# Kernel optimization log

Hardware: AMD Instinct MI355X
Metric: run time of the kernel (lower is better)

Reference implementation:

```python
import jax, jax.numpy as jnp
import numpy as np


def setup_inputs() -> dict:
    key = jax.random.key(0)
    k1, k2 = jax.random.split(key)
    B, N, D = 16, 2048, 256      # batch, tokens, token_dim
    C, K = 8, 1024               # num_codebooks, num_tokens
    x_in = jax.random.normal(k1, (B, N, D), dtype=jnp.float32)
    # torch.rand init for each VQCodebook embedding -> uniform[0,1)
    codebooks = jax.random.uniform(k2, (C, K, D), dtype=jnp.float32)
    return {"x_in": x_in, "codebooks": codebooks}


def _apply_one_codebook(x_res, emb, code_sg):
    d2 = (
        jnp.sum(x_res * x_res, axis=-1, keepdims=True)
        - 2.0 * jnp.einsum("bnd,kd->bnk", x_res, emb)
        + jnp.sum(emb * emb, axis=-1)
    )
    idx = jnp.argmin(d2, axis=-1)          # (B,N)
    z_q = emb[idx]                         # (B,N,D) gather
    if code_sg:                            # straight-through estimator
        z_q = x_res + jax.lax.stop_gradient(z_q - x_res)
    return z_q, idx


def reference(x_in, codebooks, code_sg=True):
    C = codebooks.shape[0]
    x_res = x_in
    z_q = jnp.zeros_like(x_in)
    idx_list = []
    for i in range(C):  # sequential residual dependency, loop over fixed num_codebooks
        # faithful to original: subtracts CUMULATIVE z_q each iteration
        x_res = x_res - z_q
        z_q_i, idx_i = _apply_one_codebook(x_res, codebooks[i], code_sg)
        z_q = z_q + z_q_i
        idx_list.append(idx_i)
    indices = jnp.stack(idx_list, axis=-2)  # (B, C, N)
    return z_q, indices
```

## Files before the change

kernel.cpp:

```cpp
#include <hip/hip_runtime.h>
#include <cstdint>

#define TOKENS   32768
#define DIM      256
#define KCB      1024
#define CBOOKS   8
#define NTOK     2048
#define ZQ_ELEMS (TOKENS * DIM)
#define EPS_GAP  2.0e-2f

typedef _Float16 f16x8 __attribute__((ext_vector_type(8)));
typedef float    f32x4 __attribute__((ext_vector_type(4)));

__device__ float np_pairwise_sumsq_256(const float4* a4) {
  #pragma clang fp contract(off)
  float h[2];
  for (int hh = 0; hh < 2; ++hh) {
    const float4* b = a4 + hh * 32;
    float4 v0 = b[0], v1 = b[1];
    float r0 = v0.x * v0.x, r1 = v0.y * v0.y, r2 = v0.z * v0.z, r3 = v0.w * v0.w;
    float r4 = v1.x * v1.x, r5 = v1.y * v1.y, r6 = v1.z * v1.z, r7 = v1.w * v1.w;
    for (int t = 1; t < 16; ++t) {
      float4 w0 = b[2 * t], w1 = b[2 * t + 1];
      r0 = r0 + w0.x * w0.x; r1 = r1 + w0.y * w0.y;
      r2 = r2 + w0.z * w0.z; r3 = r3 + w0.w * w0.w;
      r4 = r4 + w1.x * w1.x; r5 = r5 + w1.y * w1.y;
      r6 = r6 + w1.z * w1.z; r7 = r7 + w1.w * w1.w;
    }
    h[hh] = ((r0 + r1) + (r2 + r3)) + ((r4 + r5) + (r6 + r7));
  }
  return h[0] + h[1];
}

__device__ __forceinline__ float4 f4_muladd(float4 a, float4 b, float4 c) {
  #pragma clang fp contract(off)
  float4 r;
  r.x = a.x * b.x + c.x;
  r.y = a.y * b.y + c.y;
  r.z = a.z * b.z + c.z;
  r.w = a.w * b.w + c.w;
  return r;
}

__global__ __launch_bounds__(256) void rvq_norms_kernel(
    const float* __restrict__ cb, float* __restrict__ sume) {
  int row = blockIdx.x * 256 + threadIdx.x;
  sume[row] = np_pairwise_sumsq_256((const float4*)&cb[(size_t)row * DIM]);
}

__global__ __launch_bounds__(256) void rvq_efsplit_kernel(
    const float* __restrict__ cbc, f16x8* __restrict__ EfC,
    int* __restrict__ fix_cnt) {
  if (blockIdx.x == 0 && threadIdx.x == 0) *fix_cnt = 0;
  int gw = blockIdx.x * 4 + (threadIdx.x >> 6);
  int l  = threadIdx.x & 63;
  int row = gw * 16 + (l & 15);
  #pragma unroll
  for (int kb = 0; kb < 8; ++kb) {
    int d0 = kb * 32 + ((l >> 4) << 3);
    float4 u = *(const float4*)&cbc[(size_t)row * DIM + d0];
    float4 v = *(const float4*)&cbc[(size_t)row * DIM + d0 + 4];
    float ev[8] = {u.x, u.y, u.z, u.w, v.x, v.y, v.z, v.w};
    f16x8 hi, lo;
    #pragma unroll
    for (int i = 0; i < 8; ++i) {
      _Float16 h = (_Float16)ev[i];
      hi[i] = h; lo[i] = (_Float16)(ev[i] - (float)h);
    }
    EfC[((size_t)gw * 16 + kb) * 64 + l]     = hi;
    EfC[((size_t)gw * 16 + kb + 8) * 64 + l] = lo;
  }
}

__global__ __launch_bounds__(256, 2) void rvq_screen_kernel(
    const float* __restrict__ xr, const f16x8* __restrict__ EfC,
    const float* __restrict__ sume, int* __restrict__ idx_ws,
    int* __restrict__ fix_list, int* __restrict__ fix_cnt,
    float* __restrict__ idxf) {
  __shared__ f16x8 ldsB[2][2][8][2][64];

  const int tid  = threadIdx.x;
  const int lane = tid & 63;
  const int w    = tid >> 6;
  const int m0w  = blockIdx.x * 64 + w * 16;

  f16x8 ah[8], al[8];
  {
    const float* base = &xr[(size_t)(m0w + (lane & 15)) * DIM + ((lane >> 4) << 3)];
    #pragma unroll
    for (int kc = 0; kc < 8; ++kc) {
      float4 u = *(const float4*)(base + kc * 32);
      float4 v = *(const float4*)(base + kc * 32 + 4);
      float xv[8] = {u.x, u.y, u.z, u.w, v.x, v.y, v.z, v.w};
      #pragma unroll
      for (int i = 0; i < 8; ++i) {
        _Float16 h = (_Float16)xv[i];
        ah[kc][i] = h; al[kc][i] = (_Float16)(xv[i] - (float)h);
      }
    }
  }

  float rv1[4], rv2[4]; int ri1[4];
  #pragma unroll
  for (int r = 0; r < 4; ++r) { rv1[r] = 3.0e38f; rv2[r] = 3.0e38f; ri1[r] = 0x7fffffff; }

#define STAGE_B(BUF, NT, KCB_)                                               \
  { _Pragma("unroll")                                                        \
    for (int cc = 0; cc < 8; ++cc) {                                         \
      int p = cc * 4 + w;                                                    \
      int half = p & 1, ni = (p >> 1) & 7, kcw = p >> 4;                     \
      const f16x8* src =                                                     \
          &EfC[(((size_t)(NT) * 8 + ni) * 16 + (KCB_) + kcw + (half ? 8 : 0))\
               * 64 + lane];                                                 \
      __builtin_amdgcn_global_load_lds(                                      \
          (const __attribute__((address_space(1))) uint32_t*)src,            \
          (__attribute__((address_space(3))) uint32_t*)&ldsB[BUF][kcw][ni][half][0], \
          16, 0, 0);                                                         \
    } }

#define MFMA_CHUNK(BUF, KCB_)                                                \
  { _Pragma("unroll")                                                        \
    for (int kcw = 0; kcw < 2; ++kcw) {                                      \
      _Pragma("unroll")                                                      \
      for (int ni = 0; ni < 8; ++ni) {                                       \
        f16x8 bh = ldsB[BUF][kcw][ni][0][lane];                              \
        f16x8 bl = ldsB[BUF][kcw][ni][1][lane];                              \
        acc[ni] = __builtin_amdgcn_mfma_f32_16x16x32_f16(                    \
            ah[(KCB_) + kcw], bh, acc[ni], 0, 0, 0);                         \
        acc[ni] = __builtin_amdgcn_mfma_f32_16x16x32_f16(                    \
            al[(KCB_) + kcw], bh, acc[ni], 0, 0, 0);                         \
        acc[ni] = __builtin_amdgcn_mfma_f32_16x16x32_f16(                    \
            ah[(KCB_) + kcw], bl, acc[ni], 0, 0, 0);                         \
      }                                                                      \
    } }

  f32x4 acc[8];
  #pragma unroll
  for (int ni = 0; ni < 8; ++ni) acc[ni] = (f32x4){0.f, 0.f, 0.f, 0.f};

  STAGE_B(0, 0, 0)
  __syncthreads();

  #pragma unroll 1
  for (int ntile = 0; ntile < 8; ++ntile) {
    #pragma unroll
    for (int chunk = 0; chunk < 4; ++chunk) {
      const int buf = chunk & 1;
      if (ntile * 4 + chunk < 31) {
        int nt2  = (chunk < 3) ? ntile : ntile + 1;
        int kcb2 = ((chunk + 1) & 3) * 2;
        STAGE_B(buf ^ 1, nt2, kcb2)
      }
      MFMA_CHUNK(buf, chunk * 2)
      __syncthreads();
    }
    const int n0 = ntile * 128;
    float se[8];
    #pragma unroll
    for (int ni = 0; ni < 8; ++ni) se[ni] = sume[n0 + ni * 16 + (lane & 15)];
    #pragma unroll
    for (int r = 0; r < 4; ++r) {
      float v1 = 3.0e38f, v2 = 3.0e38f; int i1 = 0x7fffffff;
      #pragma unroll
      for (int ni = 0; ni < 8; ++ni) {
        float key = fmaf(-2.0f, acc[ni][r], se[ni]);
        int   k   = n0 + ni * 16 + (lane & 15);
        if (key < v1 || (key == v1 && k < i1)) { v2 = v1; v1 = key; i1 = k; }
        else { v2 = fminf(v2, key); }
      }
      #pragma unroll
      for (int off = 1; off < 16; off <<= 1) {
        float ov1 = __shfl_xor(v1, off, 64);
        int   oi1 = __shfl_xor(i1, off, 64);
        float ov2 = __shfl_xor(v2, off, 64);
        if (ov1 < v1 || (ov1 == v1 && oi1 < i1)) { v2 = fminf(ov2, v1); v1 = ov1; i1 = oi1; }
        else { v2 = fminf(v2, fminf(ov1, ov2)); }
      }
      if (v1 < rv1[r] || (v1 == rv1[r] && i1 < ri1[r])) {
        rv2[r] = fminf(rv1[r], v2); rv1[r] = v1; ri1[r] = i1;
      } else { rv2[r] = fminf(rv2[r], fminf(v1, v2)); }
    }
    #pragma unroll
    for (int ni = 0; ni < 8; ++ni) acc[ni] = (f32x4){0.f, 0.f, 0.f, 0.f};
  }
#undef STAGE_B
#undef MFMA_CHUNK

  if ((lane & 15) == 0) {
    #pragma unroll
    for (int r = 0; r < 4; ++r) {
      int token = m0w + (lane >> 4) * 4 + r;
      idx_ws[token] = ri1[r];
      if (rv2[r] - rv1[r] < EPS_GAP) {
        int pos = atomicAdd(fix_cnt, 1);
        fix_list[pos] = token;
      }
      int b = token >> 11, n = token & (NTOK - 1);
      idxf[(size_t)b * (CBOOKS * NTOK) + n] = (float)ri1[r];
    }
  }
}

__global__ __launch_bounds__(256, 2) void rvq_fixup_kernel(
    const float* __restrict__ xr, const float* __restrict__ cbc,
    const float* __restrict__ sume, const int* __restrict__ fix_list,
    const int* __restrict__ fix_cnt, int* __restrict__ idx_ws,
    float* __restrict__ idxf) {
  #pragma clang fp contract(off)
  __shared__ float xs[DIM];
  __shared__ float redv[4];
  __shared__ int   redi[4];
  __shared__ float sxv_sh;
  const int tid  = threadIdx.x;
  const int nfix = *fix_cnt;

  #pragma unroll 1
  for (int i = blockIdx.x; i < nfix; i += gridDim.x) {
    int token = fix_list[i];
    __syncthreads();
    if (tid < 64)
      ((float4*)xs)[tid] = ((const float4*)xr)[(size_t)token * 64 + tid];
    __syncthreads();
    if (tid < 64) {
      float s = 0.f;
      if ((tid & 63) < 16) {
        int j = tid & 7, hh = (tid >> 3) & 1;
        const float* bb = xs + hh * 128;
        float r = bb[j] * bb[j];
        #pragma unroll 1
        for (int t = 1; t < 16; ++t) r = r + bb[8 * t + j] * bb[8 * t + j];
        s = r;
      }
      #pragma unroll
      for (int off = 1; off <= 8; off <<= 1)
        s = s + __shfl_xor(s, off, 64);
      if (tid == 0) sxv_sh = s;
    }
    __syncthreads();
    float sxv = sxv_sh;
    float bv = 3.0e38f; int bi = 0x7fffffff;
    #pragma unroll 1
    for (int kk = 0; kk < 4; ++kk) {
      int k = kk * 256 + tid;
      float4 vacc = {0.f, 0.f, 0.f, 0.f};
      #pragma unroll 1
      for (int t = 0; t < 16; ++t) {
        float4 ab = vacc;
        #pragma unroll
        for (int j = 3; j >= 0; --j) {
          float4 xq = *(const float4*)&xs[t * 16 + j * 4];
          float4 eq = *(const float4*)&cbc[(size_t)k * DIM + t * 16 + j * 4];
          ab = f4_muladd(xq, eq, ab);
        }
        vacc = ab;
      }
      float dot = (vacc.x + vacc.y) + (vacc.z + vacc.w);
      float d2  = (sxv - 2.0f * dot) + sume[k];
      if (d2 < bv || (d2 == bv && k < bi)) { bv = d2; bi = k; }
    }
    #pragma unroll
    for (int off = 1; off < 64; off <<= 1) {
      float ov = __shfl_xor(bv, off, 64);
      int   oi = __shfl_xor(bi, off, 64);
      if (ov < bv || (ov == bv && oi < bi)) { bv = ov; bi = oi; }
    }
    int w = tid >> 6;
    if ((tid & 63) == 0) { redv[w] = bv; redi[w] = bi; }
    __syncthreads();
    if (tid == 0) {
      #pragma unroll
      for (int ww = 1; ww < 4; ++ww)
        if (redv[ww] < bv || (redv[ww] == bv && redi[ww] < bi)) { bv = redv[ww]; bi = redi[ww]; }
      idx_ws[token] = bi;
      int b = token >> 11, n = token & (NTOK - 1);
      idxf[(size_t)b * (CBOOKS * NTOK) + n] = (float)bi;
    }
  }
}

__global__ __launch_bounds__(256) void rvq_zq_resid_kernel(
    const float* __restrict__ xsrc, const float* __restrict__ cbc,
    const int* __restrict__ idx_ws, float* __restrict__ zq,
    float* __restrict__ xdst, int first, int last) {
  #pragma clang fp contract(off)
  int gid   = blockIdx.x * 256 + threadIdx.x;
  int token = gid >> 6;
  int q     = gid & 63;
  int idx   = idx_ws[token];
  float4 e = ((const float4*)cbc)[(size_t)idx * 64 + q];
  float4 x = ((const float4*)xsrc)[gid];
  float4 zi;
  zi.x = x.x + (e.x - x.x); zi.y = x.y + (e.y - x.y);
  zi.z = x.z + (e.z - x.z); zi.w = x.w + (e.w - x.w);
  float4 zo;
  if (first) { zo = zi; }
  else {
    float4 z = ((float4*)zq)[gid];
    zo.x = z.x + zi.x; zo.y = z.y + zi.y; zo.z = z.z + zi.z; zo.w = z.w + zi.w;
  }
  ((float4*)zq)[gid] = zo;
  if (!last) {
    float4 xn;
    xn.x = x.x - zo.x; xn.y = x.y - zo.y; xn.z = x.z - zo.z; xn.w = x.w - zo.w;
    ((float4*)xdst)[gid] = xn;
  }
}

extern "C" void kernel_launch(void* const* d_in, const int* in_sizes, int n_in,
                              void* d_out, int out_size, void* d_ws, size_t ws_size,
                              hipStream_t stream) {
  const float* x_in = (const float*)d_in[0];
  const float* cbs  = (const float*)d_in[1];
  float* zq      = (float*)d_out;
  float* idxbase = (float*)d_out + ZQ_ELEMS;

  char* ws = (char*)d_ws;
  float*  sume     = (float*)ws;
  int*    idx_ws   = (int*)(ws + (256 << 10));
  int*    fix_list = (int*)(ws + (448 << 10));
  int*    fix_cnt  = (int*)(ws + (640 << 10));
  f16x8*  EfC      = (f16x8*)(ws + (5 << 20));
  float*  xr       = (float*)(ws + (8 << 20));

  rvq_norms_kernel<<<32, 256, 0, stream>>>(cbs, sume);
  for (int c = 0; c < CBOOKS; ++c) {
    const float* src = (c == 0) ? x_in : xr;
    const float* cbc = cbs + (size_t)c * KCB * DIM;
    float* idxf = idxbase + (size_t)c * NTOK;
    rvq_efsplit_kernel<<<16, 256, 0, stream>>>(cbc, EfC, fix_cnt);
    rvq_screen_kernel<<<512, 256, 0, stream>>>(
        src, EfC, sume + (size_t)c * KCB, idx_ws, fix_list, fix_cnt, idxf);
    rvq_fixup_kernel<<<256, 256, 0, stream>>>(
        src, cbc, sume + (size_t)c * KCB, fix_list, fix_cnt, idx_ws, idxf);
    rvq_zq_resid_kernel<<<8192, 256, 0, stream>>>(
        src, cbc, idx_ws, zq, xr, c == 0, c == CBOOKS - 1);
  }
}
```

Measured before the change: 1.005 ms.

## Fuse z_q accumulation and residual update into the next screen kernel's prologue

```diff
diff --git a/kernel.cpp b/kernel.cpp
--- a/kernel.cpp
+++ b/kernel.cpp
@@ -73,10 +73,11 @@
 }
 
 __global__ __launch_bounds__(256, 2) void rvq_screen_kernel(
-    const float* __restrict__ xr, const f16x8* __restrict__ EfC,
-    const float* __restrict__ sume, int* __restrict__ idx_ws,
-    int* __restrict__ fix_list, int* __restrict__ fix_cnt,
-    float* __restrict__ idxf) {
+    const float* __restrict__ xsrc, const float* __restrict__ cbp,
+    const f16x8* __restrict__ EfC, const float* __restrict__ sume,
+    int* __restrict__ idx_ws, int* __restrict__ fix_list,
+    int* __restrict__ fix_cnt, float* __restrict__ idxf,
+    float* __restrict__ zq, float* __restrict__ xr_out, int mode) {
   __shared__ f16x8 ldsB[2][2][8][2][64];
 
   const int tid  = threadIdx.x;
@@ -86,11 +87,43 @@
 
   f16x8 ah[8], al[8];
   {
-    const float* base = &xr[(size_t)(m0w + (lane & 15)) * DIM + ((lane >> 4) << 3)];
+    #pragma clang fp contract(off)
+    const int tok   = m0w + (lane & 15);
+    const int dbase = (lane >> 4) << 3;
+    const float4* xp = (const float4*)(xsrc + (size_t)tok * DIM + dbase);
+    const float4* ep = (const float4*)(cbp + (size_t)(mode ? idx_ws[tok] : 0) * DIM + dbase);
+    const float4* zr = (const float4*)(zq + (size_t)tok * DIM + dbase);
+    float4* zw = (float4*)(zq + (size_t)tok * DIM + dbase);
+    float4* xw = (float4*)(xr_out + (size_t)tok * DIM + dbase);
     #pragma unroll
     for (int kc = 0; kc < 8; ++kc) {
-      float4 u = *(const float4*)(base + kc * 32);
-      float4 v = *(const float4*)(base + kc * 32 + 4);
+      float4 u = xp[kc * 8], v = xp[kc * 8 + 1];
+      if (mode) {
+        float4 e0 = ep[kc * 8], e1 = ep[kc * 8 + 1];
+        float4 zi0, zi1;
+        zi0.x = u.x + (e0.x - u.x); zi0.y = u.y + (e0.y - u.y);
+        zi0.z = u.z + (e0.z - u.z); zi0.w = u.w + (e0.w - u.w);
+        zi1.x = v.x + (e1.x - v.x); zi1.y = v.y + (e1.y - v.y);
+        zi1.z = v.z + (e1.z - v.z); zi1.w = v.w + (e1.w - v.w);
+        float4 zn0, zn1;
+        if (mode == 2) {
+          float4 z0 = zr[kc * 8], z1 = zr[kc * 8 + 1];
+          zn0.x = z0.x + zi0.x; zn0.y = z0.y + zi0.y;
+          zn0.z = z0.z + zi0.z; zn0.w = z0.w + zi0.w;
+          zn1.x = z1.x + zi1.x; zn1.y = z1.y + zi1.y;
+          zn1.z = z1.z + zi1.z; zn1.w = z1.w + zi1.w;
+        } else { zn0 = zi0; zn1 = zi1; }
+        zw[kc * 8]     = zn0;
+        zw[kc * 8 + 1] = zn1;
+        float4 n0, n1;
+        n0.x = u.x - zn0.x; n0.y = u.y - zn0.y;
+        n0.z = u.z - zn0.z; n0.w = u.w - zn0.w;
+        n1.x = v.x - zn1.x; n1.y = v.y - zn1.y;
+        n1.z = v.z - zn1.z; n1.w = v.w - zn1.w;
+        xw[kc * 8]     = n0;
+        xw[kc * 8 + 1] = n1;
+        u = n0; v = n1;
+      }
       float xv[8] = {u.x, u.y, u.z, u.w, v.x, v.y, v.z, v.w};
       #pragma unroll
       for (int i = 0; i < 8; ++i) {
@@ -278,10 +311,9 @@
   }
 }
 
-__global__ __launch_bounds__(256) void rvq_zq_resid_kernel(
+__global__ __launch_bounds__(256) void rvq_zq_final_kernel(
     const float* __restrict__ xsrc, const float* __restrict__ cbc,
-    const int* __restrict__ idx_ws, float* __restrict__ zq,
-    float* __restrict__ xdst, int first, int last) {
+    const int* __restrict__ idx_ws, float* __restrict__ zq) {
   #pragma clang fp contract(off)
   int gid   = blockIdx.x * 256 + threadIdx.x;
   int token = gid >> 6;
@@ -292,18 +324,10 @@
   float4 zi;
   zi.x = x.x + (e.x - x.x); zi.y = x.y + (e.y - x.y);
   zi.z = x.z + (e.z - x.z); zi.w = x.w + (e.w - x.w);
+  float4 z = ((float4*)zq)[gid];
   float4 zo;
-  if (first) { zo = zi; }
-  else {
-    float4 z = ((float4*)zq)[gid];
-    zo.x = z.x + zi.x; zo.y = z.y + zi.y; zo.z = z.z + zi.z; zo.w = z.w + zi.w;
-  }
+  zo.x = z.x + zi.x; zo.y = z.y + zi.y; zo.z = z.z + zi.z; zo.w = z.w + zi.w;
   ((float4*)zq)[gid] = zo;
-  if (!last) {
-    float4 xn;
-    xn.x = x.x - zo.x; xn.y = x.y - zo.y; xn.z = x.z - zo.z; xn.w = x.w - zo.w;
-    ((float4*)xdst)[gid] = xn;
-  }
 }
 
 extern "C" void kernel_launch(void* const* d_in, const int* in_sizes, int n_in,
@@ -324,15 +348,19 @@
 
   rvq_norms_kernel<<<32, 256, 0, stream>>>(cbs, sume);
   for (int c = 0; c < CBOOKS; ++c) {
-    const float* src = (c == 0) ? x_in : xr;
-    const float* cbc = cbs + (size_t)c * KCB * DIM;
+    const float* xsrc = (c <= 1) ? x_in : xr;
+    const float* cbp  = cbs + (size_t)(c > 0 ? c - 1 : 0) * KCB * DIM;
+    const float* cbc  = cbs + (size_t)c * KCB * DIM;
     float* idxf = idxbase + (size_t)c * NTOK;
+    int mode = (c == 0) ? 0 : (c == 1) ? 1 : 2;
     rvq_efsplit_kernel<<<16, 256, 0, stream>>>(cbc, EfC, fix_cnt);
     rvq_screen_kernel<<<512, 256, 0, stream>>>(
-        src, EfC, sume + (size_t)c * KCB, idx_ws, fix_list, fix_cnt, idxf);
+        xsrc, cbp, EfC, sume + (size_t)c * KCB, idx_ws, fix_list, fix_cnt,
+        idxf, zq, xr, mode);
     rvq_fixup_kernel<<<256, 256, 0, stream>>>(
-        src, cbc, sume + (size_t)c * KCB, fix_list, fix_cnt, idx_ws, idxf);
-    rvq_zq_resid_kernel<<<8192, 256, 0, stream>>>(
-        src, cbc, idx_ws, zq, xr, c == 0, c == CBOOKS - 1);
-  }
-}
+        (c == 0) ? x_in : xr, cbc, sume + (size_t)c * KCB,
+        fix_list, fix_cnt, idx_ws, idxf);
+  }
+  rvq_zq_final_kernel<<<8192, 256, 0, stream>>>(
+      xr, cbs + (size_t)(CBOOKS - 1) * KCB * DIM, idx_ws, zq);
+}
```

Result: faster. 976.6 us (-2.8%).
